# Kernel tuning notes

Hardware: AMD Instinct MI355X
Metric: run time of the kernel (lower is better)

The kernel has to match this reference:

```python
import jax, jax.numpy as jnp
import numpy as np

B, N, C, K = 4, 4096, 128, 16
LN_EPS = 1e-5


def knn(x, k):
    # x: [B,N,3] -> idx of k nearest (incl. self): [B,N,k]
    xx = jnp.sum(x * x, axis=2, keepdims=True)            # [B,N,1]
    inner = -2.0 * jnp.matmul(x, jnp.swapaxes(x, 1, 2))   # [B,N,N]
    pairwise = -xx - inner - jnp.swapaxes(xx, 1, 2)       # = -||xi-xj||^2
    _, idx = jax.lax.top_k(pairwise, k)                   # largest = nearest
    return idx


def index_points(points, idx):
    # points: [B,N,C], idx: [B,N,K] -> [B,N,K,C]
    return jax.vmap(lambda p, i: p[i])(points, idx)


def layer_norm(x, g, b):
    m = jnp.mean(x, axis=-1, keepdims=True)
    v = jnp.mean((x - m) ** 2, axis=-1, keepdims=True)
    return (x - m) * jax.lax.rsqrt(v + LN_EPS) * g + b


def setup_inputs() -> dict:
    key = jax.random.key(0)
    ks = jax.random.split(key, 16)
    h, q = C // 2, C // 4
    w = lambda k, s, sc: jax.random.normal(k, s, jnp.float32) * sc
    return dict(
        xyz=jax.random.normal(ks[0], (B, N, 3), jnp.float32),
        features=jax.random.normal(ks[1], (B, N, C), jnp.float32),
        geo_w1=w(ks[2], (10, h), 0.3), geo_b1=jnp.zeros((h,), jnp.float32),
        geo_g1=jnp.ones((h,), jnp.float32), geo_be1=jnp.zeros((h,), jnp.float32),
        geo_w2=w(ks[3], (h, h), 0.12), geo_b2=jnp.zeros((h,), jnp.float32),
        diff_w1=w(ks[4], (C, h), 0.09), diff_b1=jnp.zeros((h,), jnp.float32),
        diff_g1=jnp.ones((h,), jnp.float32), diff_be1=jnp.zeros((h,), jnp.float32),
        diff_w2=w(ks[5], (h, h), 0.12), diff_b2=jnp.zeros((h,), jnp.float32),
        ep_w1=w(ks[6], (C, q), 0.09), ep_b1=jnp.zeros((q,), jnp.float32),
        ep_w2=w(ks[7], (q, 1), 0.17), ep_b2=jnp.zeros((1,), jnp.float32),
        ref_w1=w(ks[8], (2 * C, C), 0.06), ref_b1=jnp.zeros((C,), jnp.float32),
        ref_g1=jnp.ones((C,), jnp.float32), ref_be1=jnp.zeros((C,), jnp.float32),
    )


def reference(xyz, features,
              geo_w1, geo_b1, geo_g1, geo_be1, geo_w2, geo_b2,
              diff_w1, diff_b1, diff_g1, diff_be1, diff_w2, diff_b2,
              ep_w1, ep_b1, ep_w2, ep_b2,
              ref_w1, ref_b1, ref_g1, ref_be1):
    # --- geometric features ---
    idx = knn(xyz, K)                                    # [B,N,K]
    neighbors = index_points(xyz, idx)                   # [B,N,K,3]
    rel_pos = neighbors - xyz[:, :, None, :]             # [B,N,K,3]
    cov = jnp.einsum('bnkc,bnkd->bncd', rel_pos, rel_pos) / K  # [B,N,3,3]
    _, eigvecs = jnp.linalg.eigh(cov)                    # ascending eigenvalues
    normal = eigvecs[..., :, 0]                          # smallest-eig direction
    curvature_dir = eigvecs[..., :, 2]                   # largest-eig direction
    mean_rel = jnp.mean(rel_pos, axis=2)                 # [B,N,3]
    mean_dist = jnp.mean(jnp.linalg.norm(rel_pos, axis=-1), axis=-1, keepdims=True)
    geo_feat = jnp.concatenate([normal, curvature_dir, mean_rel, mean_dist], axis=-1)  # [B,N,10]

    geo_h = layer_norm(geo_feat @ geo_w1 + geo_b1, geo_g1, geo_be1)
    geo_encoded = jax.nn.relu(geo_h) @ geo_w2 + geo_b2   # [B,N,C/2]

    # --- feature differences (knn recomputed as in the original) ---
    idx2 = knn(xyz, K)
    neighbor_feats = index_points(features, idx2)        # [B,N,K,C]
    feat_diff = jnp.mean(jnp.abs(features[:, :, None, :] - neighbor_feats), axis=2)  # [B,N,C]
    diff_h = layer_norm(feat_diff @ diff_w1 + diff_b1, diff_g1, diff_be1)
    diff_encoded = jax.nn.relu(diff_h) @ diff_w2 + diff_b2

    # --- edge probability + refinement ---
    edge_feat = jnp.concatenate([geo_encoded, diff_encoded], axis=-1)  # [B,N,C]
    ep_h = jax.nn.relu(edge_feat @ ep_w1 + ep_b1)
    edge_prob = jax.nn.sigmoid(ep_h @ ep_w2 + ep_b2)     # [B,N,1]

    enhanced = jnp.concatenate([features, edge_feat * edge_prob], axis=-1)  # [B,N,2C]
    refined = jax.nn.relu(layer_norm(enhanced @ ref_w1 + ref_b1, ref_g1, ref_be1))
    refined = refined + features                          # dropout in eval mode = identity
    return refined, edge_prob
```

## Files before the change

kernel.cpp:

```cpp
#include <hip/hip_runtime.h>
#include <hip/hip_bf16.h>

#define N_ 4096
#define C_ 128
#define K_ 16
#define NPT 16384

__device__ __forceinline__ float wave_sum64(float v) {
#pragma unroll
  for (int off = 32; off >= 1; off >>= 1) v += __shfl_xor(v, off, 64);
  return v;
}

__device__ __forceinline__ float grp32_sum(float v) {
  v += __shfl_xor(v, 1, 64);
  v += __shfl_xor(v, 2, 64);
  v += __shfl_xor(v, 4, 64);
  v += __shfl_xor(v, 8, 64);
  v += __shfl_xor(v, 16, 64);
  return v;
}


__device__ __forceinline__ float sign_f(float a, float b) {
  return copysignf(fabsf(a), b);
}

__device__ float lapy2_f(float x, float y) {
#pragma clang fp contract(off)
  float xa = fabsf(x), ya = fabsf(y);
  float w = fmaxf(xa, ya), z = fminf(xa, ya);
  if (z == 0.0f) return w;
  float t = z / w;
  return w * sqrtf(1.0f + t * t);
}

__device__ void lartg_f(float f, float g, float& c, float& s, float& r) {
#pragma clang fp contract(off)
  if (g == 0.0f) {
    c = 1.0f; s = 0.0f; r = f;
  } else if (f == 0.0f) {
    c = 0.0f; s = copysignf(1.0f, g); r = fabsf(g);
  } else {
    float d = sqrtf(f * f + g * g);
    c = fabsf(f) / d;
    r = sign_f(d, f);
    s = g / r;
  }
}

__device__ void laev2_f(float a, float b, float cc, float& rt1, float& rt2,
                        float& cs1, float& sn1) {
#pragma clang fp contract(off)
  float sm = a + cc;
  float df = a - cc;
  float adf = fabsf(df);
  float tb = b + b;
  float ab = fabsf(tb);
  float acmx, acmn;
  if (fabsf(a) > fabsf(cc)) { acmx = a; acmn = cc; } else { acmx = cc; acmn = a; }
  float rt;
  if (adf > ab) {
    float t = ab / adf; rt = adf * sqrtf(1.0f + t * t);
  } else if (adf < ab) {
    float t = adf / ab; rt = ab * sqrtf(1.0f + t * t);
  } else {
    rt = ab * sqrtf(2.0f);
  }
  int sgn1;
  if (sm < 0.0f) {
    rt1 = 0.5f * (sm - rt); sgn1 = -1;
    rt2 = (acmx / rt1) * acmn - (b / rt1) * b;
  } else if (sm > 0.0f) {
    rt1 = 0.5f * (sm + rt); sgn1 = 1;
    rt2 = (acmx / rt1) * acmn - (b / rt1) * b;
  } else {
    rt1 = 0.5f * rt; rt2 = -0.5f * rt; sgn1 = 1;
  }
  float cs; int sgn2;
  if (df >= 0.0f) { cs = df + rt; sgn2 = 1; } else { cs = df - rt; sgn2 = -1; }
  float acs = fabsf(cs);
  if (acs > ab) {
    float ct = -tb / cs;
    sn1 = 1.0f / sqrtf(1.0f + ct * ct);
    cs1 = ct * sn1;
  } else {
    if (ab == 0.0f) { cs1 = 1.0f; sn1 = 0.0f; }
    else {
      float tn = -cs / tb;
      cs1 = 1.0f / sqrtf(1.0f + tn * tn);
      sn1 = tn * cs1;
    }
  }
  if (sgn1 == sgn2) { float tn = cs1; cs1 = -sn1; sn1 = tn; }
}

__device__ void steqr3_f(float d[3], float e[2], float Z[3][3]) {
#pragma clang fp contract(off)
  const int n = 3;
  const float eps = 5.9604644775390625e-08f;
  const float eps2 = eps * eps;
  const float safmin = 1.17549435e-38f;
  const int nmaxit = n * 30;
  int jtot = 0;
  int l1 = 1;

  for (int og = 0; og < 16; ++og) {
    if (l1 > n) break;
    if (l1 > 1) e[l1 - 2] = 0.0f;
    int m, l, lend;
    if (l1 <= n - 1) {
      bool found = false;
      for (m = l1; m <= n - 1; ++m) {
        float tst = fabsf(e[m - 1]);
        if (tst == 0.0f) { found = true; break; }
        if (tst <= (sqrtf(fabsf(d[m - 1])) * sqrtf(fabsf(d[m]))) * eps) {
          e[m - 1] = 0.0f; found = true; break;
        }
      }
      if (!found) m = n;
    } else {
      m = n;
    }
    l = l1; lend = m; l1 = m + 1;
    if (lend == l) continue;
    if (fabsf(d[lend - 1]) < fabsf(d[l - 1])) { int t = l; l = lend; lend = t; }

    if (lend > l) {
      for (int it = 0; it < 128; ++it) {
        int mm;
        if (l != lend) {
          bool f2 = false;
          for (mm = l; mm <= lend - 1; ++mm) {
            float tst = e[mm - 1] * e[mm - 1];
            if (tst <= (eps2 * fabsf(d[mm - 1])) * fabsf(d[mm]) + safmin) { f2 = true; break; }
          }
          if (!f2) mm = lend;
        } else mm = lend;
        if (mm < lend) e[mm - 1] = 0.0f;
        float p = d[l - 1];
        if (mm == l) {
          d[l - 1] = p; ++l;
          if (l <= lend) continue;
          break;
        }
        if (mm == l + 1) {
          float rt1, rt2, cc, ss;
          laev2_f(d[l - 1], e[l - 1], d[l], rt1, rt2, cc, ss);
          for (int r = 0; r < n; ++r) {
            float temp = Z[r][l];
            Z[r][l] = cc * temp - ss * Z[r][l - 1];
            Z[r][l - 1] = ss * temp + cc * Z[r][l - 1];
          }
          d[l - 1] = rt1; d[l] = rt2; e[l - 1] = 0.0f;
          l += 2;
          if (l <= lend) continue;
          break;
        }
        if (jtot == nmaxit) break;
        ++jtot;
        float g = (d[l] - p) / (2.0f * e[l - 1]);
        float r = lapy2_f(g, 1.0f);
        g = d[mm - 1] - p + e[l - 1] / (g + sign_f(r, g));
        float s = 1.0f, c = 1.0f;
        p = 0.0f;
        float csv[2], snv[2];
        for (int i = mm - 1; i >= l; --i) {
          float f = s * e[i - 1];
          float bb = c * e[i - 1];
          lartg_f(g, f, c, s, r);
          if (i != mm - 1) e[i] = r;
          g = d[i] - p;
          r = (d[i - 1] - g) * s + 2.0f * c * bb;
          p = s * r;
          d[i] = g + p;
          g = c * r - bb;
          csv[i - l] = c;
          snv[i - l] = -s;
        }
        int mml = mm - l;
        for (int j = mml; j >= 1; --j) {
          float cc = csv[j - 1], ss = snv[j - 1];
          for (int r2 = 0; r2 < n; ++r2) {
            float temp = Z[r2][l + j - 1];
            Z[r2][l + j - 1] = cc * temp - ss * Z[r2][l + j - 2];
            Z[r2][l + j - 2] = ss * temp + cc * Z[r2][l + j - 2];
          }
        }
        d[l - 1] -= p;
        e[l - 1] = g;
      }
    } else {
      for (int it = 0; it < 128; ++it) {
        int mm;
        if (l != lend) {
          bool f2 = false;
          for (mm = l; mm >= lend + 1; --mm) {
            float tst = e[mm - 2] * e[mm - 2];
            if (tst <= (eps2 * fabsf(d[mm - 1])) * fabsf(d[mm - 2]) + safmin) { f2 = true; break; }
          }
          if (!f2) mm = lend;
        } else mm = lend;
        if (mm > lend) e[mm - 2] = 0.0f;
        float p = d[l - 1];
        if (mm == l) {
          d[l - 1] = p; --l;
          if (l >= lend) continue;
          break;
        }
        if (mm == l - 1) {
          float rt1, rt2, cc, ss;
          laev2_f(d[l - 2], e[l - 2], d[l - 1], rt1, rt2, cc, ss);
          for (int r = 0; r < n; ++r) {
            float temp = Z[r][l - 1];
            Z[r][l - 1] = cc * temp - ss * Z[r][l - 2];
            Z[r][l - 2] = ss * temp + cc * Z[r][l - 2];
          }
          d[l - 2] = rt1; d[l - 1] = rt2; e[l - 2] = 0.0f;
          l -= 2;
          if (l >= lend) continue;
          break;
        }
        if (jtot == nmaxit) break;
        ++jtot;
        float g = (d[l - 2] - p) / (2.0f * e[l - 2]);
        float r = lapy2_f(g, 1.0f);
        g = d[mm - 1] - p + e[l - 2] / (g + sign_f(r, g));
        float s = 1.0f, c = 1.0f;
        p = 0.0f;
        float csv[2], snv[2];
        for (int i = mm; i <= l - 1; ++i) {
          float f = s * e[i - 1];
          float bb = c * e[i - 1];
          lartg_f(g, f, c, s, r);
          if (i != mm) e[i - 2] = r;
          g = d[i - 1] - p;
          r = (d[i] - g) * s + 2.0f * c * bb;
          p = s * r;
          d[i - 1] = g + p;
          g = c * r - bb;
          csv[i - mm] = c;
          snv[i - mm] = s;
        }
        int lm = l - mm;
        for (int j = 1; j <= lm; ++j) {
          float cc = csv[j - 1], ss = snv[j - 1];
          for (int r2 = 0; r2 < n; ++r2) {
            float temp = Z[r2][mm + j - 1];
            Z[r2][mm + j - 1] = cc * temp - ss * Z[r2][mm + j - 2];
            Z[r2][mm + j - 2] = ss * temp + cc * Z[r2][mm + j - 2];
          }
        }
        d[l - 1] -= p;
        e[l - 2] = g;
      }
    }
  }
  for (int ii = 2; ii <= n; ++ii) {
    int i = ii - 1, k = i;
    float p = d[i - 1];
    for (int j = ii; j <= n; ++j) {
      if (d[j - 1] < p) { k = j; p = d[j - 1]; }
    }
    if (k != i) {
      d[k - 1] = d[i - 1]; d[i - 1] = p;
      for (int r = 0; r < n; ++r) {
        float t = Z[r][i - 1]; Z[r][i - 1] = Z[r][k - 1]; Z[r][k - 1] = t;
      }
    }
  }
}

__device__ void eig3_f(float A00, float A10, float A20,
                       float A11, float A21, float A22, float Z[3][3]) {
#pragma clang fp contract(off)
  float d[3], e[2];
  float tau = 0.0f, v2 = 0.0f;
  d[0] = A00;
  float xnorm = fabsf(A20);
  if (xnorm == 0.0f) {
    tau = 0.0f; v2 = 0.0f;
    e[0] = A10; d[1] = A11; e[1] = A21; d[2] = A22;
  } else {
    float beta = -sign_f(lapy2_f(A10, xnorm), A10);
    tau = (beta - A10) / beta;
    float inv = 1.0f / (A10 - beta);
    v2 = A20 * inv;
    e[0] = beta;
    float x0 = tau * A11;
    float x1 = tau * A21;
    float tmp2 = A21 * v2;
    x0 = x0 + tau * tmp2;
    x1 = x1 + (tau * v2) * A22;
    float dotv = x0 + x1 * v2;
    float aw = (-0.5f * tau) * dotv;
    float w0 = x0 + aw;
    float w1 = x1 + aw * v2;
    d[1] = (A11 - w0) - w0;
    float pq = v2 * w0;
    e[1] = (A21 - pq) - w1;
    float pr = v2 * w1;
    d[2] = (A22 - pr) - pr;
  }
  Z[0][0] = 1.0f; Z[0][1] = 0.0f; Z[0][2] = 0.0f;
  Z[1][0] = 0.0f; Z[1][1] = 1.0f; Z[1][2] = 0.0f;
  Z[2][0] = 0.0f; Z[2][1] = 0.0f; Z[2][2] = 1.0f;
  steqr3_f(d, e, Z);
  if (tau != 0.0f) {
    for (int j = 0; j < 3; ++j) {
      float sum = Z[1][j] + v2 * Z[2][j];
      float tw = tau * sum;
      Z[1][j] = Z[1][j] - tw;
      Z[2][j] = Z[2][j] - v2 * tw;
    }
  }
}

__device__ __forceinline__ unsigned long long knn_key(float qx, float qy, float qz,
                                                      float nqxx, float x, float y,
                                                      float z, int j) {
  const float dot = __fmaf_rn(qz, z, __fmaf_rn(qy, y, __fmul_rn(qx, x)));
  const float xxj =
      __fadd_rn(__fadd_rn(__fmul_rn(x, x), __fmul_rn(y, y)), __fmul_rn(z, z));
  const float inner = __fmul_rn(-2.0f, dot);
  const float pval = __fsub_rn(__fsub_rn(nqxx, inner), xxj);
  const unsigned bits = __float_as_uint(pval);
  const unsigned ordv = bits ^ (unsigned)(((int)bits >> 31) | 0x80000000);
  return ((unsigned long long)ordv << 32) | (unsigned)(4095 - j);
}

__global__ __launch_bounds__(256, 6) void knn_kernel(const float* __restrict__ xyz,
                                                     int* __restrict__ nidx_ws) {
  __shared__ float4 tile4[1024];

  const int wave = threadIdx.x >> 6;
  const int lane = threadIdx.x & 63;
  const int tid = threadIdx.x;
  const int P0 = blockIdx.x * 8;
  const int b = P0 >> 12;
  const int r0 = P0 & 4095;
  const int pbase = r0 + wave * 2;
  const float* xb = xyz + (size_t)b * (N_ * 3);

  float qx[2], qy[2], qz[2], nqxx[2];
#pragma unroll
  for (int q = 0; q < 2; ++q) {
    const int i = pbase + q;
    qx[q] = xb[3 * i]; qy[q] = xb[3 * i + 1]; qz[q] = xb[3 * i + 2];
    nqxx[q] = -__fadd_rn(__fadd_rn(__fmul_rn(qx[q], qx[q]), __fmul_rn(qy[q], qy[q])),
                         __fmul_rn(qz[q], qz[q]));
  }

  unsigned long long pk[2][4];
#pragma unroll
  for (int q = 0; q < 2; ++q)
#pragma unroll
    for (int s = 0; s < 4; ++s) pk[q][s] = 0ull;

  for (int tile = 0; tile < 4; ++tile) {
    {
      const float4* gsrc = (const float4*)(xb + tile * 3072);
      float4 a0 = gsrc[tid * 3];
      float4 a1 = gsrc[tid * 3 + 1];
      float4 a2 = gsrc[tid * 3 + 2];
      const int base = tid * 4;
      const float xx0 = __fadd_rn(__fadd_rn(__fmul_rn(a0.x, a0.x), __fmul_rn(a0.y, a0.y)), __fmul_rn(a0.z, a0.z));
      const float xx1 = __fadd_rn(__fadd_rn(__fmul_rn(a0.w, a0.w), __fmul_rn(a1.x, a1.x)), __fmul_rn(a1.y, a1.y));
      const float xx2 = __fadd_rn(__fadd_rn(__fmul_rn(a1.z, a1.z), __fmul_rn(a1.w, a1.w)), __fmul_rn(a2.x, a2.x));
      const float xx3 = __fadd_rn(__fadd_rn(__fmul_rn(a2.y, a2.y), __fmul_rn(a2.z, a2.z)), __fmul_rn(a2.w, a2.w));
      tile4[base]     = make_float4(a0.x, a0.y, a0.z, xx0);
      tile4[base + 1] = make_float4(a0.w, a1.x, a1.y, xx1);
      tile4[base + 2] = make_float4(a1.z, a1.w, a2.x, xx2);
      tile4[base + 3] = make_float4(a2.y, a2.z, a2.w, xx3);
    }
    __syncthreads();

#pragma unroll 2
    for (int tloc = 0; tloc < 16; ++tloc) {
      const int idx = tloc * 64 + lane;
      const int j = tile * 1024 + idx;
      const float4 pv = tile4[idx];
      const float x = pv.x;
      const float y = pv.y;
      const float z = pv.z;
      const float xxj = pv.w;
      const unsigned jenc = (unsigned)(4095 - j);
#pragma unroll
      for (int q = 0; q < 2; ++q) {
        const float dot =
            __fmaf_rn(qz[q], z, __fmaf_rn(qy[q], y, __fmul_rn(qx[q], x)));
        const float inner = __fmul_rn(-2.0f, dot);
        const float pval = __fsub_rn(__fsub_rn(nqxx[q], inner), xxj);
        const unsigned bits = __float_as_uint(pval);
        const unsigned ordv = bits ^ (unsigned)(((int)bits >> 31) | 0x80000000);
        const unsigned long long key = ((unsigned long long)ordv << 32) | jenc;
        const bool c3 = key > pk[q][3];
        if (__any(c3)) {
          const bool c0 = key > pk[q][0], c1 = key > pk[q][1], c2 = key > pk[q][2];
          pk[q][3] = c3 ? (c2 ? pk[q][2] : key) : pk[q][3];
          pk[q][2] = c2 ? (c1 ? pk[q][1] : key) : pk[q][2];
          pk[q][1] = c1 ? (c0 ? pk[q][0] : key) : pk[q][1];
          pk[q][0] = c0 ? key : pk[q][0];
        }
      }
    }
    __syncthreads();
  }

  int stash[2];
  int h[2] = {0, 0};
#pragma unroll
  for (int k = 0; k < K_; ++k) {
    unsigned long long v[2];
#pragma unroll
    for (int q = 0; q < 2; ++q) v[q] = pk[q][0];
#pragma unroll
    for (int off = 32; off >= 1; off >>= 1) {
#pragma unroll
      for (int q = 0; q < 2; ++q) {
        unsigned long long ov = __shfl_xor(v[q], off, 64);
        if (ov > v[q]) v[q] = ov;
      }
    }
#pragma unroll
    for (int q = 0; q < 2; ++q) {
      const int jidx = (4095 - (int)(unsigned)(v[q] & 0xFFFFFFFFull)) & (N_ - 1);
      if (lane == k) stash[q] = jidx;
      if (pk[q][0] == v[q]) {
        pk[q][0] = pk[q][1]; pk[q][1] = pk[q][2]; pk[q][2] = pk[q][3];
        pk[q][3] = 0ull;
        ++h[q];
      }
    }
  }
#pragma unroll
  for (int q = 0; q < 2; ++q) {
    if (__ballot(h[q] >= 4) != 0ull) {
      unsigned long long qq[K_];
#pragma unroll
      for (int k = 0; k < K_; ++k) qq[k] = 0ull;
      for (int t = 0; t < 64; ++t) {
        const int j = t * 64 + lane;
        const unsigned long long key = knn_key(qx[q], qy[q], qz[q], nqxx[q],
                                               xb[3 * j], xb[3 * j + 1],
                                               xb[3 * j + 2], j);
        bool c[K_];
#pragma unroll
        for (int s = 0; s < K_; ++s) c[s] = key > qq[s];
#pragma unroll
        for (int s = K_ - 1; s >= 1; --s)
          qq[s] = c[s] ? (c[s - 1] ? qq[s - 1] : key) : qq[s];
        qq[0] = c[0] ? key : qq[0];
      }
#pragma unroll
      for (int k = 0; k < K_; ++k) {
        unsigned long long v = qq[0];
#pragma unroll
        for (int off = 32; off >= 1; off >>= 1) {
          unsigned long long ov = __shfl_xor(v, off, 64);
          if (ov > v) v = ov;
        }
        const int jidx = (4095 - (int)(unsigned)(v & 0xFFFFFFFFull)) & (N_ - 1);
        if (lane == k) stash[q] = jidx;
        if (qq[0] == v) {
#pragma unroll
          for (int s = 0; s < K_ - 1; ++s) qq[s] = qq[s + 1];
          qq[K_ - 1] = 0ull;
        }
      }
    }
  }

  if (lane < K_) {
    const int pg = P0 + wave * 2;
#pragma unroll
    for (int q = 0; q < 2; ++q)
      nidx_ws[(size_t)(pg + q) * K_ + lane] = stash[q];
  }
}

__global__ __launch_bounds__(64) void eig_kernel(const float* __restrict__ xyz,
                                                 const int* __restrict__ nidx_ws,
                                                 float* __restrict__ gf_ws) {
  const int p = blockIdx.x * 64 + threadIdx.x;
  const int b = p >> 12;
  const int i = p & 4095;
  const float* xb = xyz + (size_t)b * (N_ * 3);
  const float qx = xb[3 * i];
  const float qy = xb[3 * i + 1];
  const float qz = xb[3 * i + 2];

  int nidx[K_];
#pragma unroll
  for (int k = 0; k < K_; ++k) nidx[k] = nidx_ws[(size_t)p * K_ + k];

  float c00 = 0, c01 = 0, c02 = 0, c11 = 0, c12 = 0, c22 = 0;
  float mrx = 0, mry = 0, mrz = 0, md = 0;
#pragma unroll
  for (int k = 0; k < K_; ++k) {
    const int j = nidx[k];
    const float rx = __fsub_rn(xb[3 * j], qx);
    const float ry = __fsub_rn(xb[3 * j + 1], qy);
    const float rz = __fsub_rn(xb[3 * j + 2], qz);
    c00 = __fadd_rn(c00, __fmul_rn(rx, rx));
    c01 = __fadd_rn(c01, __fmul_rn(rx, ry));
    c02 = __fadd_rn(c02, __fmul_rn(rx, rz));
    c11 = __fadd_rn(c11, __fmul_rn(ry, ry));
    c12 = __fadd_rn(c12, __fmul_rn(ry, rz));
    c22 = __fadd_rn(c22, __fmul_rn(rz, rz));
    mrx = __fadd_rn(mrx, rx);
    mry = __fadd_rn(mry, ry);
    mrz = __fadd_rn(mrz, rz);
    const float nn = __fadd_rn(__fadd_rn(__fmul_rn(rx, rx), __fmul_rn(ry, ry)),
                               __fmul_rn(rz, rz));
    md = __fadd_rn(md, sqrtf(nn));
  }
  const float s16 = 0.0625f;
  float Z[3][3];
  eig3_f(__fmul_rn(c00, s16), __fmul_rn(c01, s16), __fmul_rn(c02, s16),
         __fmul_rn(c11, s16), __fmul_rn(c12, s16), __fmul_rn(c22, s16), Z);
  float* g = gf_ws + (size_t)p * 12;
  g[0] = Z[0][0]; g[1] = Z[1][0]; g[2] = Z[2][0];
  g[3] = Z[0][2]; g[4] = Z[1][2]; g[5] = Z[2][2];
  g[6] = __fmul_rn(mrx, s16); g[7] = __fmul_rn(mry, s16);
  g[8] = __fmul_rn(mrz, s16);
  g[9] = __fmul_rn(md, s16);
}

__global__ __launch_bounds__(256) void mlp_kernel(
    const float* __restrict__ feats, const int* __restrict__ nidx_ws,
    const float* __restrict__ gf_ws,
    const float* __restrict__ geo_w1, const float* __restrict__ geo_b1,
    const float* __restrict__ geo_g1, const float* __restrict__ geo_be1,
    const float* __restrict__ geo_w2, const float* __restrict__ geo_b2,
    const float* __restrict__ diff_w1, const float* __restrict__ diff_b1,
    const float* __restrict__ diff_g1, const float* __restrict__ diff_be1,
    const float* __restrict__ diff_w2, const float* __restrict__ diff_b2,
    const float* __restrict__ ep_w1, const float* __restrict__ ep_b1,
    const float* __restrict__ ep_w2, const float* __restrict__ ep_b2,
    const float* __restrict__ ref_w1, const float* __restrict__ ref_b1,
    const float* __restrict__ ref_g1, const float* __restrict__ ref_be1,
    float* __restrict__ out, float* __restrict__ out_prob) {

  __shared__ float w[8192];
  __shared__ float fsh[16 * 128];
  __shared__ float sdif[16 * 128];
  __shared__ float ysh[16 * 64];
  __shared__ float edsh[16 * 128];
  __shared__ float insh[16 * 12];
  __shared__ int nsh[16 * 16];

  const int tid = threadIdx.x;
  const int lane = tid & 63;
  const int g = tid >> 6;
  const int P0 = blockIdx.x * 16;
  const int b = P0 >> 12;
  const int r0 = P0 & 4095;
  const float* fb = feats + (size_t)b * N_ * C_;

  if (tid < 192) insh[tid] = gf_ws[(size_t)P0 * 12 + tid];
  nsh[tid] = nidx_ws[(size_t)P0 * K_ + tid];
#pragma unroll
  for (int m = 0; m < 8; ++m)
    fsh[m * 256 + tid] = fb[(size_t)r0 * C_ + m * 256 + tid];
  if (tid < 160) ((float4*)w)[tid] = ((const float4*)geo_w1)[tid];
#pragma unroll
  for (int m = 0; m < 4; ++m)
    ((float4*)(w + 640))[m * 256 + tid] = ((const float4*)geo_w2)[m * 256 + tid];
  __syncthreads();

  {
    float acc[4] = {0, 0, 0, 0};
#pragma unroll
    for (int c = 0; c < 10; ++c) {
      const float wv = w[c * 64 + lane];
#pragma unroll
      for (int ptl = 0; ptl < 4; ++ptl)
        acc[ptl] += insh[(g * 4 + ptl) * 12 + c] * wv;
    }
#pragma unroll
    for (int ptl = 0; ptl < 4; ++ptl) {
      const int pt = g * 4 + ptl;
      float a = acc[ptl] + geo_b1[lane];
      float m = wave_sum64(a) * (1.0f / 64.0f);
      float xm = a - m;
      float var = wave_sum64(xm * xm) * (1.0f / 64.0f);
      float yv = xm * (1.0f / sqrtf(var + 1e-5f)) * geo_g1[lane] + geo_be1[lane];
      ysh[pt * 64 + lane] = fmaxf(yv, 0.0f);
    }
  }
  __syncthreads();

  float ge[4] = {0, 0, 0, 0}, de[4], prob[4];
#pragma unroll 4
  for (int c = 0; c < 64; ++c) {
    const float wv = w[640 + c * 64 + lane];
#pragma unroll
    for (int ptl = 0; ptl < 4; ++ptl)
      ge[ptl] += ysh[(g * 4 + ptl) * 64 + c] * wv;
  }
#pragma unroll
  for (int ptl = 0; ptl < 4; ++ptl) ge[ptl] += geo_b2[lane];

  {
    const int h2 = tid >> 7, c = tid & 127;
    for (int ptp = 0; ptp < 8; ++ptp) {
      const int pt = h2 * 8 + ptp;
      const float fv = fsh[pt * 128 + c];
      float s = 0.0f;
#pragma unroll
      for (int k = 0; k < K_; ++k) {
        const int j = nsh[pt * 16 + k];
        s += fabsf(fv - fb[(size_t)j * C_ + c]);
      }
      sdif[pt * 128 + c] = s * (1.0f / 16.0f);
    }
  }
  __syncthreads();
#pragma unroll
  for (int m = 0; m < 8; ++m)
    ((float4*)w)[m * 256 + tid] = ((const float4*)diff_w1)[m * 256 + tid];
  __syncthreads();

  {
    float acc[4] = {0, 0, 0, 0};
#pragma unroll 4
    for (int c = 0; c < 128; ++c) {
      const float wv = w[c * 64 + lane];
#pragma unroll
      for (int ptl = 0; ptl < 4; ++ptl)
        acc[ptl] += sdif[(g * 4 + ptl) * 128 + c] * wv;
    }
#pragma unroll
    for (int ptl = 0; ptl < 4; ++ptl) {
      const int pt = g * 4 + ptl;
      float a = acc[ptl] + diff_b1[lane];
      float m = wave_sum64(a) * (1.0f / 64.0f);
      float xm = a - m;
      float var = wave_sum64(xm * xm) * (1.0f / 64.0f);
      float yv = xm * (1.0f / sqrtf(var + 1e-5f)) * diff_g1[lane] + diff_be1[lane];
      ysh[pt * 64 + lane] = fmaxf(yv, 0.0f);
    }
  }
  __syncthreads();
#pragma unroll
  for (int m = 0; m < 4; ++m)
    ((float4*)w)[m * 256 + tid] = ((const float4*)diff_w2)[m * 256 + tid];
#pragma unroll
  for (int m = 0; m < 4; ++m)
    ((float4*)w)[1024 + m * 256 + tid] = ((const float4*)ep_w1)[m * 256 + tid];
  __syncthreads();

  {
    float acc[4] = {0, 0, 0, 0};
#pragma unroll 4
    for (int c = 0; c < 64; ++c) {
      const float wv = w[c * 64 + lane];
#pragma unroll
      for (int ptl = 0; ptl < 4; ++ptl)
        acc[ptl] += ysh[(g * 4 + ptl) * 64 + c] * wv;
    }
#pragma unroll
    for (int ptl = 0; ptl < 4; ++ptl) {
      const int pt = g * 4 + ptl;
      de[ptl] = acc[ptl] + diff_b2[lane];
      edsh[pt * 128 + lane] = ge[ptl];
      edsh[pt * 128 + 64 + lane] = de[ptl];
    }
  }
  __syncthreads();

  const int u = lane & 31;
  {
    float ea[4] = {0, 0, 0, 0};
#pragma unroll 4
    for (int c = 0; c < 128; ++c) {
      const float wv = w[4096 + c * 32 + u];
#pragma unroll
      for (int ptl = 0; ptl < 4; ++ptl)
        ea[ptl] += edsh[(g * 4 + ptl) * 128 + c] * wv;
    }
#pragma unroll
    for (int ptl = 0; ptl < 4; ++ptl) {
      float a = ea[ptl] + ep_b1[u];
      float hh = (lane < 32) ? fmaxf(a, 0.0f) * ep_w2[u] : 0.0f;
      float tsum = wave_sum64(hh) + ep_b2[0];
      prob[ptl] = 1.0f / (1.0f + expf(-tsum));
      if (lane == 0) out_prob[P0 + g * 4 + ptl] = prob[ptl];
    }
  }
  __syncthreads();
#pragma unroll
  for (int ptl = 0; ptl < 4; ++ptl) {
    const int pt = g * 4 + ptl;
    edsh[pt * 128 + lane] = ge[ptl] * prob[ptl];
    edsh[pt * 128 + 64 + lane] = de[ptl] * prob[ptl];
  }

  const int p2 = tid >> 5;
  const int ptA = p2 * 2, ptB = ptA + 1;
  const int oc4 = (tid & 31) * 4;
  float A0 = 0, A1 = 0, A2 = 0, A3 = 0;
  float B0 = 0, B1 = 0, B2 = 0, B3 = 0;
  for (int ch = 0; ch < 4; ++ch) {
    __syncthreads();
    {
      const float4* gsrc = (const float4*)(ref_w1 + ch * 8192);
#pragma unroll
      for (int m = 0; m < 8; ++m) ((float4*)w)[m * 256 + tid] = gsrc[m * 256 + tid];
    }
    __syncthreads();
    const float* eA = (ch < 2) ? (fsh + ptA * 128 + ch * 64)
                               : (edsh + ptA * 128 + (ch - 2) * 64);
    const float* eB = (ch < 2) ? (fsh + ptB * 128 + ch * 64)
                               : (edsh + ptB * 128 + (ch - 2) * 64);
#pragma unroll 4
    for (int c4 = 0; c4 < 64; c4 += 4) {
      const float4 ea = *(const float4*)(eA + c4);
      const float4 eb = *(const float4*)(eB + c4);
      const float4 w0 = *(const float4*)(w + (c4 + 0) * 128 + oc4);
      const float4 w1 = *(const float4*)(w + (c4 + 1) * 128 + oc4);
      const float4 w2 = *(const float4*)(w + (c4 + 2) * 128 + oc4);
      const float4 w3 = *(const float4*)(w + (c4 + 3) * 128 + oc4);
      A0 += ea.x * w0.x; A0 += ea.y * w1.x; A0 += ea.z * w2.x; A0 += ea.w * w3.x;
      A1 += ea.x * w0.y; A1 += ea.y * w1.y; A1 += ea.z * w2.y; A1 += ea.w * w3.y;
      A2 += ea.x * w0.z; A2 += ea.y * w1.z; A2 += ea.z * w2.z; A2 += ea.w * w3.z;
      A3 += ea.x * w0.w; A3 += ea.y * w1.w; A3 += ea.z * w2.w; A3 += ea.w * w3.w;
      B0 += eb.x * w0.x; B0 += eb.y * w1.x; B0 += eb.z * w2.x; B0 += eb.w * w3.x;
      B1 += eb.x * w0.y; B1 += eb.y * w1.y; B1 += eb.z * w2.y; B1 += eb.w * w3.y;
      B2 += eb.x * w0.z; B2 += eb.y * w1.z; B2 += eb.z * w2.z; B2 += eb.w * w3.z;
      B3 += eb.x * w0.w; B3 += eb.y * w1.w; B3 += eb.z * w2.w; B3 += eb.w * w3.w;
    }
  }

  {
    const float4 rb = *(const float4*)(ref_b1 + oc4);
    A0 += rb.x; A1 += rb.y; A2 += rb.z; A3 += rb.w;
    B0 += rb.x; B1 += rb.y; B2 += rb.z; B3 += rb.w;
    const float4 gg = *(const float4*)(ref_g1 + oc4);
    const float4 be = *(const float4*)(ref_be1 + oc4);

    const float mA = grp32_sum(A0 + A1 + A2 + A3) * (1.0f / 128.0f);
    const float dA0 = A0 - mA, dA1 = A1 - mA, dA2 = A2 - mA, dA3 = A3 - mA;
    const float vA =
        grp32_sum(dA0 * dA0 + dA1 * dA1 + dA2 * dA2 + dA3 * dA3) * (1.0f / 128.0f);
    const float rsA = 1.0f / sqrtf(vA + 1e-5f);
    const float4 resA = *(const float4*)(fsh + ptA * 128 + oc4);
    float4 yA;
    yA.x = fmaxf(dA0 * rsA * gg.x + be.x, 0.0f) + resA.x;
    yA.y = fmaxf(dA1 * rsA * gg.y + be.y, 0.0f) + resA.y;
    yA.z = fmaxf(dA2 * rsA * gg.z + be.z, 0.0f) + resA.z;
    yA.w = fmaxf(dA3 * rsA * gg.w + be.w, 0.0f) + resA.w;
    *(float4*)(out + (size_t)(P0 + ptA) * 128 + oc4) = yA;

    const float mB = grp32_sum(B0 + B1 + B2 + B3) * (1.0f / 128.0f);
    const float dB0 = B0 - mB, dB1 = B1 - mB, dB2 = B2 - mB, dB3 = B3 - mB;
    const float vB =
        grp32_sum(dB0 * dB0 + dB1 * dB1 + dB2 * dB2 + dB3 * dB3) * (1.0f / 128.0f);
    const float rsB = 1.0f / sqrtf(vB + 1e-5f);
    const float4 resB = *(const float4*)(fsh + ptB * 128 + oc4);
    float4 yB;
    yB.x = fmaxf(dB0 * rsB * gg.x + be.x, 0.0f) + resB.x;
    yB.y = fmaxf(dB1 * rsB * gg.y + be.y, 0.0f) + resB.y;
    yB.z = fmaxf(dB2 * rsB * gg.z + be.z, 0.0f) + resB.z;
    yB.w = fmaxf(dB3 * rsB * gg.w + be.w, 0.0f) + resB.w;
    *(float4*)(out + (size_t)(P0 + ptB) * 128 + oc4) = yB;
  }
}

__global__ __launch_bounds__(256) void fused_kernel(
    const float* __restrict__ xyz, const float* __restrict__ feats,
    const float* __restrict__ geo_w1, const float* __restrict__ geo_b1,
    const float* __restrict__ geo_g1, const float* __restrict__ geo_be1,
    const float* __restrict__ geo_w2, const float* __restrict__ geo_b2,
    const float* __restrict__ diff_w1, const float* __restrict__ diff_b1,
    const float* __restrict__ diff_g1, const float* __restrict__ diff_be1,
    const float* __restrict__ diff_w2, const float* __restrict__ diff_b2,
    const float* __restrict__ ep_w1, const float* __restrict__ ep_b1,
    const float* __restrict__ ep_w2, const float* __restrict__ ep_b2,
    const float* __restrict__ ref_w1, const float* __restrict__ ref_b1,
    const float* __restrict__ ref_g1, const float* __restrict__ ref_be1,
    float* __restrict__ out, float* __restrict__ out_prob) {

  __shared__ float4 tile4[1024];

  const int wave = threadIdx.x >> 6;
  const int lane = threadIdx.x & 63;
  const int tid = threadIdx.x;
  const int p = blockIdx.x * 4 + wave;
  const int b = p >> 12;
  const int i = p & 4095;
  const float* xb = xyz + (size_t)b * (N_ * 3);

  const float qx = xb[3 * i];
  const float qy = xb[3 * i + 1];
  const float qz = xb[3 * i + 2];
  const float qxx =
      __fadd_rn(__fadd_rn(__fmul_rn(qx, qx), __fmul_rn(qy, qy)), __fmul_rn(qz, qz));
  const float nqxx = -qxx;

  unsigned long long pk[4] = {0ull, 0ull, 0ull, 0ull};
  for (int tile = 0; tile < 4; ++tile) {
    {
      const float4* gsrc = (const float4*)(xb + tile * 3072);
      float4 r0v = gsrc[tid * 3];
      float4 r1 = gsrc[tid * 3 + 1];
      float4 r2 = gsrc[tid * 3 + 2];
      const int base = tid * 4;
      tile4[base]     = make_float4(r0v.x, r0v.y, r0v.z, 0.0f);
      tile4[base + 1] = make_float4(r0v.w, r1.x, r1.y, 0.0f);
      tile4[base + 2] = make_float4(r1.z, r1.w, r2.x, 0.0f);
      tile4[base + 3] = make_float4(r2.y, r2.z, r2.w, 0.0f);
    }
    __syncthreads();
#pragma unroll 4
    for (int tloc = 0; tloc < 16; ++tloc) {
      const int j = tile * 1024 + tloc * 64 + lane;
      const float4 pt = tile4[tloc * 64 + lane];
      const unsigned long long key = knn_key(qx, qy, qz, nqxx, pt.x, pt.y, pt.z, j);
      const bool c0 = key > pk[0], c1 = key > pk[1], c2 = key > pk[2], c3 = key > pk[3];
      pk[3] = c3 ? (c2 ? pk[2] : key) : pk[3];
      pk[2] = c2 ? (c1 ? pk[1] : key) : pk[2];
      pk[1] = c1 ? (c0 ? pk[0] : key) : pk[1];
      pk[0] = c0 ? key : pk[0];
    }
    __syncthreads();
  }

  int nidx[K_];
  int h = 0;
#pragma unroll
  for (int k = 0; k < K_; ++k) {
    unsigned long long v = pk[0];
#pragma unroll
    for (int off = 32; off >= 1; off >>= 1) {
      unsigned long long ov = __shfl_xor(v, off, 64);
      if (ov > v) v = ov;
    }
    nidx[k] = (4095 - (int)(unsigned)(v & 0xFFFFFFFFull)) & (N_ - 1);
    if (pk[0] == v) {
      pk[0] = pk[1]; pk[1] = pk[2]; pk[2] = pk[3]; pk[3] = 0ull;
      ++h;
    }
  }
  if (__ballot(h >= 4) != 0ull) {
    unsigned long long q[K_];
#pragma unroll
    for (int k = 0; k < K_; ++k) q[k] = 0ull;
    for (int t = 0; t < 64; ++t) {
      const int j = t * 64 + lane;
      const unsigned long long key =
          knn_key(qx, qy, qz, nqxx, xb[3 * j], xb[3 * j + 1], xb[3 * j + 2], j);
      bool c[K_];
#pragma unroll
      for (int s = 0; s < K_; ++s) c[s] = key > q[s];
#pragma unroll
      for (int s = K_ - 1; s >= 1; --s)
        q[s] = c[s] ? (c[s - 1] ? q[s - 1] : key) : q[s];
      q[0] = c[0] ? key : q[0];
    }
#pragma unroll
    for (int k = 0; k < K_; ++k) {
      unsigned long long v = q[0];
#pragma unroll
      for (int off = 32; off >= 1; off >>= 1) {
        unsigned long long ov = __shfl_xor(v, off, 64);
        if (ov > v) v = ov;
      }
      nidx[k] = (4095 - (int)(unsigned)(v & 0xFFFFFFFFull)) & (N_ - 1);
      if (q[0] == v) {
#pragma unroll
        for (int s = 0; s < K_ - 1; ++s) q[s] = q[s + 1];
        q[K_ - 1] = 0ull;
      }
    }
  }

  float c00 = 0, c01 = 0, c02 = 0, c11 = 0, c12 = 0, c22 = 0;
  float mrx = 0, mry = 0, mrz = 0, md = 0;
#pragma unroll
  for (int k = 0; k < K_; ++k) {
    const int j = nidx[k];
    const float rx = __fsub_rn(xb[3 * j], qx);
    const float ry = __fsub_rn(xb[3 * j + 1], qy);
    const float rz = __fsub_rn(xb[3 * j + 2], qz);
    c00 = __fadd_rn(c00, __fmul_rn(rx, rx));
    c01 = __fadd_rn(c01, __fmul_rn(rx, ry));
    c02 = __fadd_rn(c02, __fmul_rn(rx, rz));
    c11 = __fadd_rn(c11, __fmul_rn(ry, ry));
    c12 = __fadd_rn(c12, __fmul_rn(ry, rz));
    c22 = __fadd_rn(c22, __fmul_rn(rz, rz));
    mrx = __fadd_rn(mrx, rx);
    mry = __fadd_rn(mry, ry);
    mrz = __fadd_rn(mrz, rz);
    const float nn = __fadd_rn(__fadd_rn(__fmul_rn(rx, rx), __fmul_rn(ry, ry)),
                               __fmul_rn(rz, rz));
    md = __fadd_rn(md, sqrtf(nn));
  }
  const float s16 = 0.0625f;
  float Z[3][3];
  eig3_f(__fmul_rn(c00, s16), __fmul_rn(c01, s16), __fmul_rn(c02, s16),
         __fmul_rn(c11, s16), __fmul_rn(c12, s16), __fmul_rn(c22, s16), Z);
  float gf[10];
  gf[0] = Z[0][0]; gf[1] = Z[1][0]; gf[2] = Z[2][0];
  gf[3] = Z[0][2]; gf[4] = Z[1][2]; gf[5] = Z[2][2];
  gf[6] = __fmul_rn(mrx, s16); gf[7] = __fmul_rn(mry, s16);
  gf[8] = __fmul_rn(mrz, s16);
  gf[9] = __fmul_rn(md, s16);

  float acc = 0.0f;
#pragma unroll
  for (int ii = 0; ii < 10; ++ii) acc += gf[ii] * geo_w1[ii * 64 + lane];
  acc += geo_b1[lane];
  float yr;
  {
    float m = wave_sum64(acc) * (1.0f / 64.0f);
    float xm = acc - m;
    float var = wave_sum64(xm * xm) * (1.0f / 64.0f);
    float yv = xm * (1.0f / sqrtf(var + 1e-5f)) * geo_g1[lane] + geo_be1[lane];
    yr = fmaxf(yv, 0.0f);
  }
  float ge = 0.0f;
#pragma unroll 8
  for (int jj = 0; jj < 64; ++jj) ge += __shfl(yr, jj, 64) * geo_w2[jj * 64 + lane];
  ge += geo_b2[lane];

  const float* fb = feats + (size_t)b * N_ * C_;
  const float* fi = fb + (size_t)i * C_;
  const float f0 = fi[lane];
  const float f1 = fi[64 + lane];
  float s0 = 0.0f, s1 = 0.0f;
#pragma unroll
  for (int k = 0; k < K_; ++k) {
    const float* fj = fb + (size_t)nidx[k] * C_;
    s0 += fabsf(f0 - fj[lane]);
    s1 += fabsf(f1 - fj[64 + lane]);
  }
  s0 *= (1.0f / 16.0f);
  s1 *= (1.0f / 16.0f);
  float acc2 = 0.0f;
#pragma unroll 8
  for (int c = 0; c < 64; ++c) acc2 += __shfl(s0, c, 64) * diff_w1[c * 64 + lane];
#pragma unroll 8
  for (int c = 64; c < 128; ++c) acc2 += __shfl(s1, c - 64, 64) * diff_w1[c * 64 + lane];
  acc2 += diff_b1[lane];
  float yr2;
  {
    float m = wave_sum64(acc2) * (1.0f / 64.0f);
    float xm = acc2 - m;
    float var = wave_sum64(xm * xm) * (1.0f / 64.0f);
    float yv = xm * (1.0f / sqrtf(var + 1e-5f)) * diff_g1[lane] + diff_be1[lane];
    yr2 = fmaxf(yv, 0.0f);
  }
  float de = 0.0f;
#pragma unroll 8
  for (int jj = 0; jj < 64; ++jj) de += __shfl(yr2, jj, 64) * diff_w2[jj * 64 + lane];
  de += diff_b2[lane];

  {
    const int u = lane & 31;
    float a = 0.0f;
#pragma unroll 8
    for (int c = 0; c < 64; ++c) a += __shfl(ge, c, 64) * ep_w1[c * 32 + u];
#pragma unroll 8
    for (int c = 64; c < 128; ++c) a += __shfl(de, c - 64, 64) * ep_w1[c * 32 + u];
    a += ep_b1[u];
    float hh = (lane < 32) ? fmaxf(a, 0.0f) * ep_w2[u] : 0.0f;
    float tsum = wave_sum64(hh) + ep_b2[0];
    float prob = 1.0f / (1.0f + expf(-tsum));

    const float gep = ge * prob;
    const float dep = de * prob;
    float a0 = 0.0f, a1 = 0.0f;
#pragma unroll 4
    for (int c = 0; c < 64; ++c) {
      float ec = __shfl(f0, c, 64);
      a0 += ec * ref_w1[c * 128 + lane];
      a1 += ec * ref_w1[c * 128 + 64 + lane];
    }
#pragma unroll 4
    for (int c = 64; c < 128; ++c) {
      float ec = __shfl(f1, c - 64, 64);
      a0 += ec * ref_w1[c * 128 + lane];
      a1 += ec * ref_w1[c * 128 + 64 + lane];
    }
#pragma unroll 4
    for (int c = 128; c < 192; ++c) {
      float ec = __shfl(gep, c - 128, 64);
      a0 += ec * ref_w1[c * 128 + lane];
      a1 += ec * ref_w1[c * 128 + 64 + lane];
    }
#pragma unroll 4
    for (int c = 192; c < 256; ++c) {
      float ec = __shfl(dep, c - 192, 64);
      a0 += ec * ref_w1[c * 128 + lane];
      a1 += ec * ref_w1[c * 128 + 64 + lane];
    }
    a0 += ref_b1[lane];
    a1 += ref_b1[64 + lane];
    float mm2 = wave_sum64(a0 + a1) * (1.0f / 128.0f);
    float d0 = a0 - mm2, d1 = a1 - mm2;
    float var2 = wave_sum64(d0 * d0 + d1 * d1) * (1.0f / 128.0f);
    float rs = 1.0f / sqrtf(var2 + 1e-5f);
    float y0 = d0 * rs * ref_g1[lane] + ref_be1[lane];
    float y1 = d1 * rs * ref_g1[64 + lane] + ref_be1[64 + lane];
    y0 = fmaxf(y0, 0.0f) + f0;
    y1 = fmaxf(y1, 0.0f) + f1;
    out[(size_t)p * 128 + lane] = y0;
    out[(size_t)p * 128 + 64 + lane] = y1;
    if (lane == 0) out_prob[p] = prob;
  }
}

extern "C" void kernel_launch(void* const* d_in, const int* in_sizes, int n_in,
                              void* d_out, int out_size, void* d_ws, size_t ws_size,
                              hipStream_t stream) {
  const float* xyz = (const float*)d_in[0];
  const float* features = (const float*)d_in[1];
  const float* geo_w1 = (const float*)d_in[2];
  const float* geo_b1 = (const float*)d_in[3];
  const float* geo_g1 = (const float*)d_in[4];
  const float* geo_be1 = (const float*)d_in[5];
  const float* geo_w2 = (const float*)d_in[6];
  const float* geo_b2 = (const float*)d_in[7];
  const float* diff_w1 = (const float*)d_in[8];
  const float* diff_b1 = (const float*)d_in[9];
  const float* diff_g1 = (const float*)d_in[10];
  const float* diff_be1 = (const float*)d_in[11];
  const float* diff_w2 = (const float*)d_in[12];
  const float* diff_b2 = (const float*)d_in[13];
  const float* ep_w1 = (const float*)d_in[14];
  const float* ep_b1 = (const float*)d_in[15];
  const float* ep_w2 = (const float*)d_in[16];
  const float* ep_b2 = (const float*)d_in[17];
  const float* ref_w1 = (const float*)d_in[18];
  const float* ref_b1 = (const float*)d_in[19];
  const float* ref_g1 = (const float*)d_in[20];
  const float* ref_be1 = (const float*)d_in[21];

  float* out = (float*)d_out;
  float* out_prob = out + (size_t)NPT * C_;

  if (ws_size >= (size_t)(2 * 1024 * 1024)) {
    int* nidx_ws = (int*)d_ws;
    float* gf_ws = (float*)((char*)d_ws + (1u << 20));
    knn_kernel<<<dim3(NPT / 8), dim3(256), 0, stream>>>(xyz, nidx_ws);
    eig_kernel<<<dim3(NPT / 64), dim3(64), 0, stream>>>(xyz, nidx_ws, gf_ws);
    mlp_kernel<<<dim3(NPT / 16), dim3(256), 0, stream>>>(
        features, nidx_ws, gf_ws, geo_w1, geo_b1, geo_g1, geo_be1, geo_w2,
        geo_b2, diff_w1, diff_b1, diff_g1, diff_be1, diff_w2, diff_b2, ep_w1,
        ep_b1, ep_w2, ep_b2, ref_w1, ref_b1, ref_g1, ref_be1, out, out_prob);
  } else {
    fused_kernel<<<dim3(NPT / 4), dim3(256), 0, stream>>>(
        xyz, features, geo_w1, geo_b1, geo_g1, geo_be1, geo_w2, geo_b2,
        diff_w1, diff_b1, diff_g1, diff_be1, diff_w2, diff_b2, ep_w1, ep_b1,
        ep_w2, ep_b2, ref_w1, ref_b1, ref_g1, ref_be1, out, out_prob);
  }
}
```

Before: 318.5 us.

## Transpose MLP weights in shared memory with padding and vectorize gathers

Weight matrices are stored transposed and padded in LDS (stride 68/132) so each lane reads float4 runs of its own output column, and activations are read as broadcast float4. The neighbor feature gather now loads float4 per thread across channels instead of scalar loads. This is meant to cut LDS instruction count and global load instructions in the MLP stage, at the cost of strided scatter stores when staging weights and a slightly larger shared buffer.

After: 367.7 us. 1.15x slower.

```diff
diff --git a/kernel.cpp b/kernel.cpp
--- a/kernel.cpp
+++ b/kernel.cpp
@@ -542,7 +542,7 @@
     const float* __restrict__ ref_g1, const float* __restrict__ ref_be1,
     float* __restrict__ out, float* __restrict__ out_prob) {
 
-  __shared__ float w[8192];
+  __shared__ float w[8576];
   __shared__ float fsh[16 * 128];
   __shared__ float sdif[16 * 128];
   __shared__ float ysh[16 * 64];
@@ -565,8 +565,18 @@
     fsh[m * 256 + tid] = fb[(size_t)r0 * C_ + m * 256 + tid];
   if (tid < 160) ((float4*)w)[tid] = ((const float4*)geo_w1)[tid];
 #pragma unroll
-  for (int m = 0; m < 4; ++m)
-    ((float4*)(w + 640))[m * 256 + tid] = ((const float4*)geo_w2)[m * 256 + tid];
+  for (int m = 0; m < 4; ++m) {
+    const int f = m * 256 + tid;
+    const float4 v = ((const float4*)geo_w2)[f];
+    const int g0 = 4 * f;
+    const int c = g0 >> 6;
+    const int o = g0 & 63;
+    float* base = w + 640;
+    base[(o + 0) * 68 + c] = v.x;
+    base[(o + 1) * 68 + c] = v.y;
+    base[(o + 2) * 68 + c] = v.z;
+    base[(o + 3) * 68 + c] = v.w;
+  }
   __syncthreads();
 
   {
@@ -592,44 +602,66 @@
   __syncthreads();
 
   float ge[4] = {0, 0, 0, 0}, de[4], prob[4];
-#pragma unroll 4
-  for (int c = 0; c < 64; ++c) {
-    const float wv = w[640 + c * 64 + lane];
-#pragma unroll
-    for (int ptl = 0; ptl < 4; ++ptl)
-      ge[ptl] += ysh[(g * 4 + ptl) * 64 + c] * wv;
+#pragma unroll
+  for (int c4 = 0; c4 < 64; c4 += 4) {
+    const float4 wv = *(const float4*)(w + 640 + lane * 68 + c4);
+#pragma unroll
+    for (int ptl = 0; ptl < 4; ++ptl) {
+      const float4 yv = *(const float4*)(ysh + (g * 4 + ptl) * 64 + c4);
+      ge[ptl] += yv.x * wv.x; ge[ptl] += yv.y * wv.y;
+      ge[ptl] += yv.z * wv.z; ge[ptl] += yv.w * wv.w;
+    }
   }
 #pragma unroll
   for (int ptl = 0; ptl < 4; ++ptl) ge[ptl] += geo_b2[lane];
 
   {
-    const int h2 = tid >> 7, c = tid & 127;
-    for (int ptp = 0; ptp < 8; ++ptp) {
-      const int pt = h2 * 8 + ptp;
-      const float fv = fsh[pt * 128 + c];
-      float s = 0.0f;
-#pragma unroll
+    const int grp = tid >> 5;
+    const int c4 = (tid & 31) * 4;
+#pragma unroll
+    for (int pp = 0; pp < 2; ++pp) {
+      const int pt = grp * 2 + pp;
+      const float4 fv = *(const float4*)(fsh + pt * 128 + c4);
+      float s0 = 0, s1 = 0, s2 = 0, s3 = 0;
       for (int k = 0; k < K_; ++k) {
         const int j = nsh[pt * 16 + k];
-        s += fabsf(fv - fb[(size_t)j * C_ + c]);
-      }
-      sdif[pt * 128 + c] = s * (1.0f / 16.0f);
+        const float4 a = *(const float4*)(fb + (size_t)j * C_ + c4);
+        s0 += fabsf(fv.x - a.x);
+        s1 += fabsf(fv.y - a.y);
+        s2 += fabsf(fv.z - a.z);
+        s3 += fabsf(fv.w - a.w);
+      }
+      const float sc = 1.0f / 16.0f;
+      *(float4*)(sdif + pt * 128 + c4) =
+          make_float4(s0 * sc, s1 * sc, s2 * sc, s3 * sc);
     }
   }
   __syncthreads();
 #pragma unroll
-  for (int m = 0; m < 8; ++m)
-    ((float4*)w)[m * 256 + tid] = ((const float4*)diff_w1)[m * 256 + tid];
+  for (int m = 0; m < 8; ++m) {
+    const int f = m * 256 + tid;
+    const float4 v = ((const float4*)diff_w1)[f];
+    const int g0 = 4 * f;
+    const int c = g0 >> 6;
+    const int o = g0 & 63;
+    w[(o + 0) * 132 + c] = v.x;
+    w[(o + 1) * 132 + c] = v.y;
+    w[(o + 2) * 132 + c] = v.z;
+    w[(o + 3) * 132 + c] = v.w;
+  }
   __syncthreads();
 
   {
     float acc[4] = {0, 0, 0, 0};
-#pragma unroll 4
-    for (int c = 0; c < 128; ++c) {
-      const float wv = w[c * 64 + lane];
-#pragma unroll
-      for (int ptl = 0; ptl < 4; ++ptl)
-        acc[ptl] += sdif[(g * 4 + ptl) * 128 + c] * wv;
+#pragma unroll
+    for (int c4 = 0; c4 < 128; c4 += 4) {
+      const float4 wv = *(const float4*)(w + lane * 132 + c4);
+#pragma unroll
+      for (int ptl = 0; ptl < 4; ++ptl) {
+        const float4 sv = *(const float4*)(sdif + (g * 4 + ptl) * 128 + c4);
+        acc[ptl] += sv.x * wv.x; acc[ptl] += sv.y * wv.y;
+        acc[ptl] += sv.z * wv.z; acc[ptl] += sv.w * wv.w;
+      }
     }
 #pragma unroll
     for (int ptl = 0; ptl < 4; ++ptl) {
@@ -644,21 +676,43 @@
   }
   __syncthreads();
 #pragma unroll
-  for (int m = 0; m < 4; ++m)
-    ((float4*)w)[m * 256 + tid] = ((const float4*)diff_w2)[m * 256 + tid];
-#pragma unroll
-  for (int m = 0; m < 4; ++m)
-    ((float4*)w)[1024 + m * 256 + tid] = ((const float4*)ep_w1)[m * 256 + tid];
+  for (int m = 0; m < 4; ++m) {
+    const int f = m * 256 + tid;
+    const float4 v = ((const float4*)diff_w2)[f];
+    const int g0 = 4 * f;
+    const int c = g0 >> 6;
+    const int o = g0 & 63;
+    w[(o + 0) * 68 + c] = v.x;
+    w[(o + 1) * 68 + c] = v.y;
+    w[(o + 2) * 68 + c] = v.z;
+    w[(o + 3) * 68 + c] = v.w;
+  }
+#pragma unroll
+  for (int m = 0; m < 4; ++m) {
+    const int f = m * 256 + tid;
+    const float4 v = ((const float4*)ep_w1)[f];
+    const int g0 = 4 * f;
+    const int c = g0 >> 5;
+    const int o = g0 & 31;
+    float* base = w + 4352;
+    base[(o + 0) * 132 + c] = v.x;
+    base[(o + 1) * 132 + c] = v.y;
+    base[(o + 2) * 132 + c] = v.z;
+    base[(o + 3) * 132 + c] = v.w;
+  }
   __syncthreads();
 
   {
     float acc[4] = {0, 0, 0, 0};
-#pragma unroll 4
-    for (int c = 0; c < 64; ++c) {
-      const float wv = w[c * 64 + lane];
-#pragma unroll
-      for (int ptl = 0; ptl < 4; ++ptl)
-        acc[ptl] += ysh[(g * 4 + ptl) * 64 + c] * wv;
+#pragma unroll
+    for (int c4 = 0; c4 < 64; c4 += 4) {
+      const float4 wv = *(const float4*)(w + lane * 68 + c4);
+#pragma unroll
+      for (int ptl = 0; ptl < 4; ++ptl) {
+        const float4 yv = *(const float4*)(ysh + (g * 4 + ptl) * 64 + c4);
+        acc[ptl] += yv.x * wv.x; acc[ptl] += yv.y * wv.y;
+        acc[ptl] += yv.z * wv.z; acc[ptl] += yv.w * wv.w;
+      }
     }
 #pragma unroll
     for (int ptl = 0; ptl < 4; ++ptl) {
@@ -673,12 +727,15 @@
   const int u = lane & 31;
   {
     float ea[4] = {0, 0, 0, 0};
-#pragma unroll 4
-    for (int c = 0; c < 128; ++c) {
-      const float wv = w[4096 + c * 32 + u];
-#pragma unroll
-      for (int ptl = 0; ptl < 4; ++ptl)
-        ea[ptl] += edsh[(g * 4 + ptl) * 128 + c] * wv;
+#pragma unroll
+    for (int c4 = 0; c4 < 128; c4 += 4) {
+      const float4 wv = *(const float4*)(w + 4352 + u * 132 + c4);
+#pragma unroll
+      for (int ptl = 0; ptl < 4; ++ptl) {
+        const float4 ev = *(const float4*)(edsh + (g * 4 + ptl) * 128 + c4);
+        ea[ptl] += ev.x * wv.x; ea[ptl] += ev.y * wv.y;
+        ea[ptl] += ev.z * wv.z; ea[ptl] += ev.w * wv.w;
+      }
     }
 #pragma unroll
     for (int ptl = 0; ptl < 4; ++ptl) {
```
